# Performance work log

Hardware: AMD Instinct MI355X
Metric: run time of the kernel (lower is better)

Reference implementation:

```python
import jax, jax.numpy as jnp
import numpy as np

NEG_INF = -9e15  # matches the -9000000000000000.0 mask constant in the torch code
ALPHA = 0.2      # LeakyReLU negative slope


def setup_inputs() -> dict:
    key = jax.random.key(0)
    ks = jax.random.split(key, 8)
    N, F = 8192, 256
    h = jax.random.normal(ks[0], (N, F), dtype=jnp.float32)
    adj = jax.random.randint(ks[1], (N, N), 0, 2).astype(jnp.float32)
    W = jax.random.normal(ks[2], (F, F), dtype=jnp.float32) * 0.05
    a = jax.random.normal(ks[3], (2 * F, 1), dtype=jnp.float32) * 0.05
    w_ih = jax.random.normal(ks[4], (3 * F, F), dtype=jnp.float32) * 0.05
    w_hh = jax.random.normal(ks[5], (3 * F, F), dtype=jnp.float32) * 0.05
    b_ih = jax.random.normal(ks[6], (3 * F,), dtype=jnp.float32) * 0.05
    b_hh = jax.random.normal(ks[7], (3 * F,), dtype=jnp.float32) * 0.05
    return {"h": h, "adj": adj, "W": W, "a": a,
            "w_ih": w_ih, "w_hh": w_hh, "b_ih": b_ih, "b_hh": b_hh}


def reference(h, adj, W, a, w_ih, w_hh, b_ih, b_hh):
    F_out = W.shape[1]
    Wh = h @ W  # [N, F]
    # a_input @ a decomposes exactly: e_ij = leakyrelu(Wh_i . a[:F] + Wh_j . a[F:])
    src = Wh @ a[:F_out]   # [N, 1]
    dst = Wh @ a[F_out:]   # [N, 1]
    e = jax.nn.leaky_relu(src + dst.T, ALPHA)          # [N, N]
    att = jnp.where(adj > 0, e, NEG_INF)
    att = jax.nn.softmax(att, axis=1)                   # dropout: eval mode (identity)
    h_prime = att @ Wh                                  # [N, F]
    # torch GRUCell(h_prime, h)
    gi = h_prime @ w_ih.T + b_ih                        # [N, 3F]
    gh = h @ w_hh.T + b_hh
    i_r, i_z, i_n = jnp.split(gi, 3, axis=1)
    h_r, h_z, h_n = jnp.split(gh, 3, axis=1)
    r = jax.nn.sigmoid(i_r + h_r)
    z = jax.nn.sigmoid(i_z + h_z)
    n = jnp.tanh(i_n + r * h_n)
    return (1.0 - z) * n + z * h
```

## Files before the change

### kernel.cpp

```cpp
#include <hip/hip_runtime.h>

typedef __attribute__((ext_vector_type(8))) short bf16x8;
typedef __attribute__((ext_vector_type(4))) float f32x4;
typedef unsigned short u16;

#define NN 8192
#define FD 256

__device__ __forceinline__ u16 f2bf(float f) {
  union { float f; unsigned u; } v; v.f = f;
  unsigned r = v.u + 0x7FFF + ((v.u >> 16) & 1);
  return (u16)(r >> 16);
}
__device__ __forceinline__ float bf2f(u16 u) {
  union { unsigned u; float f; } v; v.u = ((unsigned)u) << 16;
  return v.f;
}

__global__ __launch_bounds__(256) void k_wh(const float* __restrict__ h,
                                            const float* __restrict__ W,
                                            u16* __restrict__ whT) {
  int tid = threadIdx.x;
  int lane = tid & 63;
  int wv = tid >> 6;
  int r0 = blockIdx.x * 64 + (wv >> 1) * 32;
  int c0 = blockIdx.y * 64 + (wv & 1) * 32;
  int lr = lane & 15;
  int q = lane >> 4;

  f32x4 acc[2][2] = {};
  for (int kk = 0; kk < FD; kk += 32) {
    int kb = kk + q * 8;
    bf16x8 a[2], b[2];
#pragma unroll
    for (int m = 0; m < 2; m++) {
      const float* p = h + (size_t)(r0 + m * 16 + lr) * FD + kb;
      f32x4 x0 = *(const f32x4*)p;
      f32x4 x1 = *(const f32x4*)(p + 4);
      bf16x8 t;
      t[0] = (short)f2bf(x0[0]); t[1] = (short)f2bf(x0[1]);
      t[2] = (short)f2bf(x0[2]); t[3] = (short)f2bf(x0[3]);
      t[4] = (short)f2bf(x1[0]); t[5] = (short)f2bf(x1[1]);
      t[6] = (short)f2bf(x1[2]); t[7] = (short)f2bf(x1[3]);
      a[m] = t;
    }
#pragma unroll
    for (int n = 0; n < 2; n++) {
      int col = c0 + n * 16 + lr;
      const float* p = W + (size_t)kb * FD + col;
      bf16x8 t;
#pragma unroll
      for (int e = 0; e < 8; e++) t[e] = (short)f2bf(p[(size_t)e * FD]);
      b[n] = t;
    }
#pragma unroll
    for (int m = 0; m < 2; m++)
#pragma unroll
      for (int n = 0; n < 2; n++)
        acc[m][n] = __builtin_amdgcn_mfma_f32_16x16x32_bf16(a[m], b[n], acc[m][n], 0, 0, 0);
  }
#pragma unroll
  for (int m = 0; m < 2; m++)
#pragma unroll
    for (int n = 0; n < 2; n++) {
      int gc = c0 + n * 16 + lr;
      int gr = r0 + m * 16 + q * 4;
      ushort4 st;
      st.x = f2bf(acc[m][n][0]);
      st.y = f2bf(acc[m][n][1]);
      st.z = f2bf(acc[m][n][2]);
      st.w = f2bf(acc[m][n][3]);
      *(ushort4*)(whT + (size_t)gc * NN + gr) = st;
    }
}

__global__ __launch_bounds__(256) void k_cast(const float* __restrict__ h,
                                              const float* __restrict__ wih,
                                              const float* __restrict__ whh,
                                              u16* __restrict__ hb,
                                              u16* __restrict__ wihb,
                                              u16* __restrict__ whhb) {
  int g = blockIdx.x * 256 + threadIdx.x;
  const int hG = NN * FD / 4;
  const int wG = 768 * FD / 4;
  const float* sp;
  u16* dp;
  int off;
  if (g < hG) { sp = h; dp = hb; off = g; }
  else if (g < hG + wG) { sp = wih; dp = wihb; off = g - hG; }
  else { sp = whh; dp = whhb; off = g - hG - wG; }
  f32x4 x = *(const f32x4*)(sp + (size_t)off * 4);
  ushort4 y;
  y.x = f2bf(x[0]); y.y = f2bf(x[1]); y.z = f2bf(x[2]); y.w = f2bf(x[3]);
  *(ushort4*)(dp + (size_t)off * 4) = y;
}

__global__ __launch_bounds__(256) void k_srcdst(const u16* __restrict__ whT,
                                                const float* __restrict__ a,
                                                float* __restrict__ src,
                                                float* __restrict__ dst) {
  __shared__ float p1[4][64];
  __shared__ float p2[4][64];
  int lane = threadIdx.x & 63;
  int wv = threadIdx.x >> 6;
  int i = blockIdx.x * 64 + lane;
  float s1 = 0.f, s2 = 0.f;
#pragma unroll 4
  for (int f = wv * 64; f < wv * 64 + 64; f++) {
    float wh = bf2f(whT[(size_t)f * NN + i]);
    s1 += wh * a[f];
    s2 += wh * a[256 + f];
  }
  p1[wv][lane] = s1;
  p2[wv][lane] = s2;
  __syncthreads();
  if (threadIdx.x < 64) {
    int ii = blockIdx.x * 64 + threadIdx.x;
    src[ii] = p1[0][threadIdx.x] + p1[1][threadIdx.x] + p1[2][threadIdx.x] + p1[3][threadIdx.x];
    dst[ii] = p2[0][threadIdx.x] + p2[1][threadIdx.x] + p2[2][threadIdx.x] + p2[3][threadIdx.x];
  }
}

__global__ __launch_bounds__(512) void k_att(const float* __restrict__ adj,
                                             const u16* __restrict__ whT,
                                             const float* __restrict__ src,
                                             const float* __restrict__ dst,
                                             u16* __restrict__ hpb) {
  __shared__ u16 Pl[2][32][72];
  __shared__ float lred[32];
  int tid = threadIdx.x;
  int i0 = blockIdx.x * 32;
  int sr = tid >> 4;
  int sc = (tid & 15) * 4;
  const float* adjRow = adj + (size_t)(i0 + sr) * NN;
  float srcv = src[i0 + sr];
  float lsum = 0.f;
  int lane = tid & 63;
  int wv = tid >> 6;
  int c0 = wv * 32;
  int lr = lane & 15;
  int q = lane >> 4;
  f32x4 acc[2][2] = {};
  f32x4 ra0, rd0, ra1, rd1;

#define LOADR(S, A, D)                                   \
  {                                                      \
    int j = (S) * 64 + sc;                               \
    A = *(const f32x4*)(adjRow + j);                     \
    D = *(const f32x4*)(dst + j);                        \
  }
#define PSTG(A, D, B)                                                   \
  {                                                                     \
    float p0, p1, p2, p3;                                               \
    { float x = srcv + D[0]; x = fmaxf(x, 0.2f * x); p0 = A[0] * __expf(x); } \
    { float x = srcv + D[1]; x = fmaxf(x, 0.2f * x); p1 = A[1] * __expf(x); } \
    { float x = srcv + D[2]; x = fmaxf(x, 0.2f * x); p2 = A[2] * __expf(x); } \
    { float x = srcv + D[3]; x = fmaxf(x, 0.2f * x); p3 = A[3] * __expf(x); } \
    lsum += (p0 + p1) + (p2 + p3);                                      \
    ushort4 st;                                                         \
    st.x = f2bf(p0); st.y = f2bf(p1); st.z = f2bf(p2); st.w = f2bf(p3); \
    *(ushort4*)&Pl[B][sr][sc] = st;                                     \
  }
#define CMP(S, B)                                                                              \
  {                                                                                            \
    _Pragma("unroll")                                                                          \
    for (int kk = 0; kk < 2; kk++) {                                                           \
      bf16x8 aF0 = *(const bf16x8*)&Pl[B][lr][kk * 32 + q * 8];                                \
      bf16x8 aF1 = *(const bf16x8*)&Pl[B][16 + lr][kk * 32 + q * 8];                           \
      bf16x8 bF0 = *(const bf16x8*)(whT + (size_t)(c0 + lr) * NN + (S) * 64 + kk * 32 + q * 8);\
      bf16x8 bF1 = *(const bf16x8*)(whT + (size_t)(c0 + 16 + lr) * NN + (S) * 64 + kk * 32 + q * 8); \
      acc[0][0] = __builtin_amdgcn_mfma_f32_16x16x32_bf16(aF0, bF0, acc[0][0], 0, 0, 0);       \
      acc[0][1] = __builtin_amdgcn_mfma_f32_16x16x32_bf16(aF0, bF1, acc[0][1], 0, 0, 0);       \
      acc[1][0] = __builtin_amdgcn_mfma_f32_16x16x32_bf16(aF1, bF0, acc[1][0], 0, 0, 0);       \
      acc[1][1] = __builtin_amdgcn_mfma_f32_16x16x32_bf16(aF1, bF1, acc[1][1], 0, 0, 0);       \
    }                                                                                          \
  }

  const int NS = NN / 64;
  LOADR(0, ra0, rd0);
  LOADR(1, ra1, rd1);
  PSTG(ra0, rd0, 0);
  __syncthreads();
  for (int s2 = 0; s2 < NS; s2 += 2) {
    if (s2 + 2 < NS) LOADR(s2 + 2, ra0, rd0);
    PSTG(ra1, rd1, 1);
    CMP(s2, 0);
    __syncthreads();
    if (s2 + 3 < NS) LOADR(s2 + 3, ra1, rd1);
    if (s2 + 2 < NS) PSTG(ra0, rd0, 0);
    CMP(s2 + 1, 1);
    __syncthreads();
  }
#pragma unroll
  for (int m = 1; m < 16; m <<= 1) lsum += __shfl_xor(lsum, m);
  if ((tid & 15) == 0) lred[sr] = lsum;
  __syncthreads();
#pragma unroll
  for (int m = 0; m < 2; m++) {
#pragma unroll
    for (int j = 0; j < 4; j++) {
      int rl = m * 16 + q * 4 + j;
      float inv = 1.0f / lred[rl];
#pragma unroll
      for (int n = 0; n < 2; n++) {
        int col = c0 + n * 16 + lr;
        hpb[(size_t)(i0 + rl) * FD + col] = f2bf(acc[m][n][j] * inv);
      }
    }
  }
#undef LOADR
#undef PSTG
#undef CMP
}

__global__ __launch_bounds__(256) void k_gru(const u16* __restrict__ hpb,
                                             const u16* __restrict__ hb,
                                             const u16* __restrict__ wihb,
                                             const u16* __restrict__ whhb,
                                             const float* __restrict__ bih,
                                             const float* __restrict__ bhh,
                                             const float* __restrict__ h,
                                             float* __restrict__ out) {
  int tid = threadIdx.x;
  int lane = tid & 63;
  int wv = tid >> 6;
  int i0 = blockIdx.x * 32;
  int lr = lane & 15;
  int q = lane >> 4;
  int c = blockIdx.y * 64 + wv * 16 + lr;
  f32x4 gi[3][2] = {};
  f32x4 gh[3][2] = {};
  for (int kk = 0; kk < FD; kk += 32) {
    int kb = kk + q * 8;
    bf16x8 ap[2], ah[2], bi[3], bh[3];
#pragma unroll
    for (int m = 0; m < 2; m++) {
      ap[m] = *(const bf16x8*)(hpb + (size_t)(i0 + m * 16 + lr) * FD + kb);
      ah[m] = *(const bf16x8*)(hb + (size_t)(i0 + m * 16 + lr) * FD + kb);
    }
#pragma unroll
    for (int g = 0; g < 3; g++) {
      bi[g] = *(const bf16x8*)(wihb + (size_t)(g * 256 + c) * FD + kb);
      bh[g] = *(const bf16x8*)(whhb + (size_t)(g * 256 + c) * FD + kb);
    }
#pragma unroll
    for (int g = 0; g < 3; g++)
#pragma unroll
      for (int m = 0; m < 2; m++) {
        gi[g][m] = __builtin_amdgcn_mfma_f32_16x16x32_bf16(ap[m], bi[g], gi[g][m], 0, 0, 0);
        gh[g][m] = __builtin_amdgcn_mfma_f32_16x16x32_bf16(ah[m], bh[g], gh[g][m], 0, 0, 0);
      }
  }
  float bir = bih[c], biz = bih[256 + c], bin = bih[512 + c];
  float bhr = bhh[c], bhz = bhh[256 + c], bhn = bhh[512 + c];
#pragma unroll
  for (int m = 0; m < 2; m++)
#pragma unroll
    for (int j = 0; j < 4; j++) {
      int row = i0 + m * 16 + q * 4 + j;
      float rv = gi[0][m][j] + bir + gh[0][m][j] + bhr;
      float zv = gi[1][m][j] + biz + gh[1][m][j] + bhz;
      float r = 1.f / (1.f + __expf(-rv));
      float z = 1.f / (1.f + __expf(-zv));
      float nx = gi[2][m][j] + bin + r * (gh[2][m][j] + bhn);
      float n = 1.f - 2.f / (__expf(2.f * nx) + 1.f);
      float hv = h[(size_t)row * FD + c];
      out[(size_t)row * FD + c] = (1.f - z) * n + z * hv;
    }
}

extern "C" void kernel_launch(void* const* d_in, const int* in_sizes, int n_in,
                              void* d_out, int out_size, void* d_ws, size_t ws_size,
                              hipStream_t stream) {
  const float* h   = (const float*)d_in[0];
  const float* adj = (const float*)d_in[1];
  const float* W   = (const float*)d_in[2];
  const float* a   = (const float*)d_in[3];
  const float* wih = (const float*)d_in[4];
  const float* whh = (const float*)d_in[5];
  const float* bih = (const float*)d_in[6];
  const float* bhh = (const float*)d_in[7];
  float* out = (float*)d_out;

  char* ws = (char*)d_ws;
  u16* whT  = (u16*)(ws);
  u16* hpb  = (u16*)(ws + 4194304);
  u16* hb   = (u16*)(ws + 8388608);
  u16* wihb = (u16*)(ws + 12582912);
  u16* whhb = (u16*)(ws + 12976128);
  float* srcv = (float*)(ws + 13369344);
  float* dstv = (float*)(ws + 13402112);

  k_wh<<<dim3(128, 4), 256, 0, stream>>>(h, W, whT);
  k_cast<<<2432, 256, 0, stream>>>(h, wih, whh, hb, wihb, whhb);
  k_srcdst<<<128, 256, 0, stream>>>(whT, a, srcv, dstv);
  k_att<<<256, 512, 0, stream>>>(adj, whT, srcv, dstv, hpb);
  k_gru<<<dim3(256, 4), 256, 0, stream>>>(hpb, hb, wihb, whhb, bih, bhh, h, out);
}
```

Baseline: 257.8 us.

## Fuse src/dst projection into Wh GEMM and restructure attention kernel as split-K

```diff
diff --git a/kernel.cpp b/kernel.cpp
--- a/kernel.cpp
+++ b/kernel.cpp
@@ -12,14 +12,13 @@
   unsigned r = v.u + 0x7FFF + ((v.u >> 16) & 1);
   return (u16)(r >> 16);
 }
-__device__ __forceinline__ float bf2f(u16 u) {
-  union { unsigned u; float f; } v; v.u = ((unsigned)u) << 16;
-  return v.f;
-}
 
 __global__ __launch_bounds__(256) void k_wh(const float* __restrict__ h,
                                             const float* __restrict__ W,
-                                            u16* __restrict__ whT) {
+                                            const float* __restrict__ a,
+                                            u16* __restrict__ whT,
+                                            float* __restrict__ src,
+                                            float* __restrict__ dst) {
   int tid = threadIdx.x;
   int lane = tid & 63;
   int wv = tid >> 6;
@@ -31,7 +30,7 @@
   f32x4 acc[2][2] = {};
   for (int kk = 0; kk < FD; kk += 32) {
     int kb = kk + q * 8;
-    bf16x8 a[2], b[2];
+    bf16x8 av[2], bv[2];
 #pragma unroll
     for (int m = 0; m < 2; m++) {
       const float* p = h + (size_t)(r0 + m * 16 + lr) * FD + kb;
@@ -42,7 +41,7 @@
       t[2] = (short)f2bf(x0[2]); t[3] = (short)f2bf(x0[3]);
       t[4] = (short)f2bf(x1[0]); t[5] = (short)f2bf(x1[1]);
       t[6] = (short)f2bf(x1[2]); t[7] = (short)f2bf(x1[3]);
-      a[m] = t;
+      av[m] = t;
     }
 #pragma unroll
     for (int n = 0; n < 2; n++) {
@@ -51,13 +50,13 @@
       bf16x8 t;
 #pragma unroll
       for (int e = 0; e < 8; e++) t[e] = (short)f2bf(p[(size_t)e * FD]);
-      b[n] = t;
+      bv[n] = t;
     }
 #pragma unroll
     for (int m = 0; m < 2; m++)
 #pragma unroll
       for (int n = 0; n < 2; n++)
-        acc[m][n] = __builtin_amdgcn_mfma_f32_16x16x32_bf16(a[m], b[n], acc[m][n], 0, 0, 0);
+        acc[m][n] = __builtin_amdgcn_mfma_f32_16x16x32_bf16(av[m], bv[n], acc[m][n], 0, 0, 0);
   }
 #pragma unroll
   for (int m = 0; m < 2; m++)
@@ -71,6 +70,25 @@
       st.z = f2bf(acc[m][n][2]);
       st.w = f2bf(acc[m][n][3]);
       *(ushort4*)(whT + (size_t)gc * NN + gr) = st;
+    }
+  float aA0 = a[c0 + lr], aA1 = a[c0 + 16 + lr];
+  float aB0 = a[256 + c0 + lr], aB1 = a[256 + c0 + 16 + lr];
+#pragma unroll
+  for (int m = 0; m < 2; m++)
+#pragma unroll
+    for (int j = 0; j < 4; j++) {
+      float s1 = acc[m][0][j] * aA0 + acc[m][1][j] * aA1;
+      float s2 = acc[m][0][j] * aB0 + acc[m][1][j] * aB1;
+#pragma unroll
+      for (int sh = 1; sh < 16; sh <<= 1) {
+        s1 += __shfl_xor(s1, sh);
+        s2 += __shfl_xor(s2, sh);
+      }
+      if (lr == 0) {
+        int row = r0 + m * 16 + q * 4 + j;
+        atomicAdd(&src[row], s1);
+        atomicAdd(&dst[row], s2);
+      }
     }
 }
 
@@ -95,122 +113,110 @@
   *(ushort4*)(dp + (size_t)off * 4) = y;
 }
 
-__global__ __launch_bounds__(256) void k_srcdst(const u16* __restrict__ whT,
-                                                const float* __restrict__ a,
-                                                float* __restrict__ src,
-                                                float* __restrict__ dst) {
-  __shared__ float p1[4][64];
-  __shared__ float p2[4][64];
-  int lane = threadIdx.x & 63;
-  int wv = threadIdx.x >> 6;
-  int i = blockIdx.x * 64 + lane;
-  float s1 = 0.f, s2 = 0.f;
-#pragma unroll 4
-  for (int f = wv * 64; f < wv * 64 + 64; f++) {
-    float wh = bf2f(whT[(size_t)f * NN + i]);
-    s1 += wh * a[f];
-    s2 += wh * a[256 + f];
-  }
-  p1[wv][lane] = s1;
-  p2[wv][lane] = s2;
-  __syncthreads();
-  if (threadIdx.x < 64) {
-    int ii = blockIdx.x * 64 + threadIdx.x;
-    src[ii] = p1[0][threadIdx.x] + p1[1][threadIdx.x] + p1[2][threadIdx.x] + p1[3][threadIdx.x];
-    dst[ii] = p2[0][threadIdx.x] + p2[1][threadIdx.x] + p2[2][threadIdx.x] + p2[3][threadIdx.x];
-  }
-}
-
-__global__ __launch_bounds__(512) void k_att(const float* __restrict__ adj,
-                                             const u16* __restrict__ whT,
-                                             const float* __restrict__ src,
-                                             const float* __restrict__ dst,
-                                             u16* __restrict__ hpb) {
-  __shared__ u16 Pl[2][32][72];
-  __shared__ float lred[32];
+__global__ __launch_bounds__(256, 2) void k_att(const float* __restrict__ adj,
+                                                const u16* __restrict__ whT,
+                                                const float* __restrict__ src,
+                                                const float* __restrict__ dst,
+                                                u16* __restrict__ hpb) {
+  __shared__ f32x4 red[2][16][64];
+  __shared__ float lred[4][16];
   int tid = threadIdx.x;
-  int i0 = blockIdx.x * 32;
-  int sr = tid >> 4;
-  int sc = (tid & 15) * 4;
-  const float* adjRow = adj + (size_t)(i0 + sr) * NN;
-  float srcv = src[i0 + sr];
-  float lsum = 0.f;
   int lane = tid & 63;
-  int wv = tid >> 6;
-  int c0 = wv * 32;
+  int w = tid >> 6;
   int lr = lane & 15;
   int q = lane >> 4;
-  f32x4 acc[2][2] = {};
-  f32x4 ra0, rd0, ra1, rd1;
-
-#define LOADR(S, A, D)                                   \
-  {                                                      \
-    int j = (S) * 64 + sc;                               \
-    A = *(const f32x4*)(adjRow + j);                     \
-    D = *(const f32x4*)(dst + j);                        \
-  }
-#define PSTG(A, D, B)                                                   \
-  {                                                                     \
-    float p0, p1, p2, p3;                                               \
-    { float x = srcv + D[0]; x = fmaxf(x, 0.2f * x); p0 = A[0] * __expf(x); } \
-    { float x = srcv + D[1]; x = fmaxf(x, 0.2f * x); p1 = A[1] * __expf(x); } \
-    { float x = srcv + D[2]; x = fmaxf(x, 0.2f * x); p2 = A[2] * __expf(x); } \
-    { float x = srcv + D[3]; x = fmaxf(x, 0.2f * x); p3 = A[3] * __expf(x); } \
-    lsum += (p0 + p1) + (p2 + p3);                                      \
-    ushort4 st;                                                         \
-    st.x = f2bf(p0); st.y = f2bf(p1); st.z = f2bf(p2); st.w = f2bf(p3); \
-    *(ushort4*)&Pl[B][sr][sc] = st;                                     \
-  }
-#define CMP(S, B)                                                                              \
-  {                                                                                            \
-    _Pragma("unroll")                                                                          \
-    for (int kk = 0; kk < 2; kk++) {                                                           \
-      bf16x8 aF0 = *(const bf16x8*)&Pl[B][lr][kk * 32 + q * 8];                                \
-      bf16x8 aF1 = *(const bf16x8*)&Pl[B][16 + lr][kk * 32 + q * 8];                           \
-      bf16x8 bF0 = *(const bf16x8*)(whT + (size_t)(c0 + lr) * NN + (S) * 64 + kk * 32 + q * 8);\
-      bf16x8 bF1 = *(const bf16x8*)(whT + (size_t)(c0 + 16 + lr) * NN + (S) * 64 + kk * 32 + q * 8); \
-      acc[0][0] = __builtin_amdgcn_mfma_f32_16x16x32_bf16(aF0, bF0, acc[0][0], 0, 0, 0);       \
-      acc[0][1] = __builtin_amdgcn_mfma_f32_16x16x32_bf16(aF0, bF1, acc[0][1], 0, 0, 0);       \
-      acc[1][0] = __builtin_amdgcn_mfma_f32_16x16x32_bf16(aF1, bF0, acc[1][0], 0, 0, 0);       \
-      acc[1][1] = __builtin_amdgcn_mfma_f32_16x16x32_bf16(aF1, bF1, acc[1][1], 0, 0, 0);       \
-    }                                                                                          \
-  }
-
-  const int NS = NN / 64;
-  LOADR(0, ra0, rd0);
-  LOADR(1, ra1, rd1);
-  PSTG(ra0, rd0, 0);
+  int i0 = blockIdx.x * 16;
+
+  const float* adjP = adj + (size_t)(i0 + lr) * NN + w * 2048 + q * 8;
+  const float* dstP = dst + w * 2048 + q * 8;
+  const u16* wp = whT + (size_t)lr * NN + w * 2048 + q * 8;
+  float srcv = src[i0 + lr];
+
+  f32x4 acc[16] = {};
+  float lsum = 0.f;
+
+  f32x4 ca0 = *(const f32x4*)(adjP);
+  f32x4 ca1 = *(const f32x4*)(adjP + 4);
+  f32x4 cd0 = *(const f32x4*)(dstP);
+  f32x4 cd1 = *(const f32x4*)(dstP + 4);
+
+#pragma unroll 2
+  for (int t = 0; t < 64; t++) {
+    float p[8];
+#pragma unroll
+    for (int e = 0; e < 4; e++) {
+      float x = srcv + cd0[e];
+      x = fmaxf(x, 0.2f * x);
+      p[e] = ca0[e] * __expf(x);
+    }
+#pragma unroll
+    for (int e = 0; e < 4; e++) {
+      float x = srcv + cd1[e];
+      x = fmaxf(x, 0.2f * x);
+      p[4 + e] = ca1[e] * __expf(x);
+    }
+    if (t < 63) {
+      ca0 = *(const f32x4*)(adjP + (t + 1) * 32);
+      ca1 = *(const f32x4*)(adjP + (t + 1) * 32 + 4);
+      cd0 = *(const f32x4*)(dstP + (t + 1) * 32);
+      cd1 = *(const f32x4*)(dstP + (t + 1) * 32 + 4);
+    }
+    lsum += ((p[0] + p[1]) + (p[2] + p[3])) + ((p[4] + p[5]) + (p[6] + p[7]));
+    bf16x8 A;
+#pragma unroll
+    for (int e = 0; e < 8; e++) A[e] = (short)f2bf(p[e]);
+    const u16* wq = wp + t * 32;
+#pragma unroll
+    for (int cf = 0; cf < 16; cf++) {
+      bf16x8 B = *(const bf16x8*)(wq + (size_t)cf * 16 * NN);
+      acc[cf] = __builtin_amdgcn_mfma_f32_16x16x32_bf16(A, B, acc[cf], 0, 0, 0);
+    }
+  }
+
+  lsum += __shfl_xor(lsum, 16);
+  lsum += __shfl_xor(lsum, 32);
+  if (lane < 16) lred[w][lane] = lsum;
+
+  if (w == 1) {
+#pragma unroll
+    for (int cf = 0; cf < 16; cf++) red[0][cf][lane] = acc[cf];
+  }
+  if (w == 3) {
+#pragma unroll
+    for (int cf = 0; cf < 16; cf++) red[1][cf][lane] = acc[cf];
+  }
   __syncthreads();
-  for (int s2 = 0; s2 < NS; s2 += 2) {
-    if (s2 + 2 < NS) LOADR(s2 + 2, ra0, rd0);
-    PSTG(ra1, rd1, 1);
-    CMP(s2, 0);
-    __syncthreads();
-    if (s2 + 3 < NS) LOADR(s2 + 3, ra1, rd1);
-    if (s2 + 2 < NS) PSTG(ra0, rd0, 0);
-    CMP(s2 + 1, 1);
-    __syncthreads();
-  }
-#pragma unroll
-  for (int m = 1; m < 16; m <<= 1) lsum += __shfl_xor(lsum, m);
-  if ((tid & 15) == 0) lred[sr] = lsum;
+  if (w == 0) {
+#pragma unroll
+    for (int cf = 0; cf < 16; cf++) acc[cf] += red[0][cf][lane];
+  }
+  if (w == 2) {
+#pragma unroll
+    for (int cf = 0; cf < 16; cf++) acc[cf] += red[1][cf][lane];
+  }
   __syncthreads();
-#pragma unroll
-  for (int m = 0; m < 2; m++) {
-#pragma unroll
-    for (int j = 0; j < 4; j++) {
-      int rl = m * 16 + q * 4 + j;
-      float inv = 1.0f / lred[rl];
-#pragma unroll
-      for (int n = 0; n < 2; n++) {
-        int col = c0 + n * 16 + lr;
-        hpb[(size_t)(i0 + rl) * FD + col] = f2bf(acc[m][n][j] * inv);
+  if (w == 2) {
+#pragma unroll
+    for (int cf = 0; cf < 16; cf++) red[0][cf][lane] = acc[cf];
+  }
+  __syncthreads();
+  if (w == 0) {
+    float inv[4];
+#pragma unroll
+    for (int jj = 0; jj < 4; jj++) {
+      int row = q * 4 + jj;
+      inv[jj] = 1.0f / (((lred[0][row] + lred[1][row]) + (lred[2][row] + lred[3][row])));
+    }
+#pragma unroll
+    for (int cf = 0; cf < 16; cf++) {
+      f32x4 v = acc[cf] + red[0][cf][lane];
+#pragma unroll
+      for (int jj = 0; jj < 4; jj++) {
+        int row = i0 + q * 4 + jj;
+        hpb[(size_t)row * FD + cf * 16 + lr] = f2bf(v[jj] * inv[jj]);
       }
     }
   }
-#undef LOADR
-#undef PSTG
-#undef CMP
 }
 
 __global__ __launch_bounds__(256) void k_gru(const u16* __restrict__ hpb,
@@ -291,9 +297,9 @@
   float* srcv = (float*)(ws + 13369344);
   float* dstv = (float*)(ws + 13402112);
 
-  k_wh<<<dim3(128, 4), 256, 0, stream>>>(h, W, whT);
+  hipMemsetAsync(ws + 13369344, 0, 65536, stream);
+  k_wh<<<dim3(128, 4), 256, 0, stream>>>(h, W, a, whT, srcv, dstv);
   k_cast<<<2432, 256, 0, stream>>>(h, wih, whh, hb, wihb, whhb);
-  k_srcdst<<<128, 256, 0, stream>>>(whT, a, srcv, dstv);
-  k_att<<<256, 512, 0, stream>>>(adj, whT, srcv, dstv, hpb);
+  k_att<<<512, 256, 0, stream>>>(adj, whT, srcv, dstv, hpb);
   k_gru<<<dim3(256, 4), 256, 0, stream>>>(hpb, hb, wihb, whhb, bih, bhh, h, out);
 }
```

Result: slower. 352.6 us (+36.8%).
